# Performance work log

Measured on AMD Instinct MI355X. Metric: run time of the kernel, lower is better.

## Reference

```python
import jax, jax.numpy as jnp
import numpy as np

B, O, D = 4096, 256, 256  # batch, size_out (rules), size_in (features)


def setup_inputs() -> dict:
    key = jax.random.key(0)
    k1, k2, k3, k4, k5 = jax.random.split(key, 5)
    return {
        "x": jax.random.normal(k1, (B, D), dtype=jnp.float32),
        "scales": jax.random.normal(k2, (O, D), dtype=jnp.float32),
        # strict upper triangle holds the packed rot vectors (original inits them to zeros;
        # small values keep the quadratic form well conditioned)
        "rots": jax.random.normal(k3, (O, D, D), dtype=jnp.float32) * 0.02,
        "centroids": jax.random.normal(k4, (O, D, 1), dtype=jnp.float32),
        "b": jax.random.uniform(k5, (O,), dtype=jnp.float32, minval=0.5, maxval=1.5),
    }


def reference(x, scales, rots, centroids, b):
    # Build symmetric transform A[o] = diag(scales[o]) + triu(rots[o],1) + triu(rots[o],1)^T
    # (equivalent to the loop of diag_embed(r_i, i+1) + mirrored lower diagonal).
    upper = jnp.triu(rots, 1)                                   # [O,D,D]
    A = upper + jnp.swapaxes(upper, -1, -2)
    A = A + jnp.eye(D, dtype=scales.dtype) * scales[:, None, :]  # diag_embed(scales)
    # Augmented affine map: mul[o,i,b'] = A[o] @ x[b'] + centroid[o,i]; const row dropped
    # since only the first size_in rows feed the norm.
    y = jnp.einsum('bj,oij->boi', x, A) + centroids[..., 0][None, :, :]  # [B,O,D]
    rx = jnp.sqrt(jnp.sum(y * y, axis=-1))                      # L2 norm over D -> [B,O]
    return 1.0 / (1.0 + rx ** (2.0 * b))                        # bell membership [B,O]
```

## Files before the change

### kernel.cpp

```cpp
#include <hip/hip_runtime.h>
#include <cstdint>
#include <cmath>

#define Bn 4096
#define Dn 256
#define On 256

typedef __bf16 v8bf __attribute__((ext_vector_type(8)));
typedef float  v4f  __attribute__((ext_vector_type(4)));
typedef unsigned short us8 __attribute__((ext_vector_type(8)));

__device__ __forceinline__ unsigned short f2bf(float f) {
    unsigned int u = __builtin_bit_cast(unsigned int, f);
    unsigned int r = (u + 0x7fffu + ((u >> 16) & 1u)) >> 16;
    return (unsigned short)r;
}

__device__ __forceinline__ void gl_lds16(const void* g, void* l) {
    __builtin_amdgcn_global_load_lds(
        (const __attribute__((address_space(1))) void*)(uintptr_t)g,
        (__attribute__((address_space(3))) void*)(uintptr_t)l, 16, 0, 0);
}

__global__ __launch_bounds__(256) void prep(
    const float* __restrict__ scales, const float* __restrict__ rots,
    const float* __restrict__ x, unsigned short* __restrict__ Ap,
    unsigned short* __restrict__ xb) {
    const int bid = blockIdx.x;
    const int tid = threadIdx.x;

    if (bid >= 2560) {
        const int cb = bid - 2560;
#pragma unroll
        for (int s = 0; s < 4; ++s) {
            const int i = cb * 4096 + s * 1024 + tid * 4;
            const float4 v = *(const float4*)(x + i);
            ushort4 u;
            u.x = f2bf(v.x); u.y = f2bf(v.y); u.z = f2bf(v.z); u.w = f2bf(v.w);
            *(ushort4*)(xb + i) = u;
        }
        return;
    }

    static const int TI[10] = {0, 0, 0, 0, 1, 1, 1, 2, 2, 3};
    static const int TJ[10] = {0, 1, 2, 3, 1, 2, 3, 2, 3, 3};
    const int o  = bid / 10;
    const int p  = bid - o * 10;
    const int ti = TI[p], tj = TJ[p];

    __shared__ float t[64][68];
    const float* src = rots + (size_t)o * Dn * Dn + (size_t)(ti * 64) * Dn + tj * 64;
#pragma unroll
    for (int s = 0; s < 4; ++s) {
        const int idx = s * 256 + tid;
        const int r = idx >> 4, c = (idx & 15) * 4;
        const float4 v = *(const float4*)(src + r * Dn + c);
        *(float4*)&t[r][c] = v;
    }
    __syncthreads();

#pragma unroll
    for (int it = 0; it < 2; ++it) {
        const int slot = it * 256 + tid;
        const int bk = slot >> 6, L = slot & 63;
        const int quad = L >> 4, frow = L & 15;
        const int sl = bk >> 1, kl = bk & 1;
        const int r = sl * 16 + frow, c = kl * 32 + quad * 8;
        float v[8];
        if (ti == tj) {
#pragma unroll
            for (int q = 0; q < 8; ++q) {
                const int cc = c + q;
                v[q] = (r < cc) ? t[r][cc]
                     : ((r > cc) ? t[cc][r] : scales[o * Dn + ti * 64 + r]);
            }
        } else {
            const float4 a = *(const float4*)&t[r][c];
            const float4 b = *(const float4*)&t[r][c + 4];
            v[0] = a.x; v[1] = a.y; v[2] = a.z; v[3] = a.w;
            v[4] = b.x; v[5] = b.y; v[6] = b.z; v[7] = b.w;
        }
        us8 u;
#pragma unroll
        for (int q = 0; q < 8; ++q) u[q] = f2bf(v[q]);
        const size_t off = ((size_t)((o * 16 + ti * 4 + sl) * 8 + tj * 2 + kl)) * 512 + L * 8;
        *(us8*)(Ap + off) = u;
    }

    if (ti != tj) {
#pragma unroll
        for (int it = 0; it < 2; ++it) {
            const int slot = it * 256 + tid;
            const int bk = slot >> 6, L = slot & 63;
            const int quad = L >> 4, frow = L & 15;
            const int sl = bk >> 1, kl = bk & 1;
            const int r = sl * 16 + frow, c = kl * 32 + quad * 8;
            us8 u;
#pragma unroll
            for (int q = 0; q < 8; ++q) u[q] = f2bf(t[c + q][r]);
            const size_t off = ((size_t)((o * 16 + tj * 4 + sl) * 8 + ti * 2 + kl)) * 512 + L * 8;
            *(us8*)(Ap + off) = u;
        }
    }
}

__global__ __launch_bounds__(256, 3) void fuzzy_main(
    const unsigned short* __restrict__ Ap, const unsigned short* __restrict__ xb,
    const float* __restrict__ cent, const float* __restrict__ bvals,
    float* __restrict__ out) {
    __shared__ __align__(16) unsigned short Xs[4][64 * 64];
    __shared__ float ssbuf[4][64];
    __shared__ float centL[Dn];

    const int tid  = threadIdx.x;
    const int lane = tid & 63;
    const int wv   = tid >> 6;
    const int Lb = blockIdx.x;
    const int o  = (Lb & 7) * 32 + (Lb >> 9);
    const int b0 = ((Lb >> 3) & 63) * 64;

    centL[tid] = cent[o * Dn + tid];

    const int frow = lane & 15, quad = lane >> 4, f3 = lane & 7;
    const int lr = lane >> 3, ls = lane & 7;
    const int ksw = (ls ^ lr) * 8;

#pragma unroll
    for (int c = 0; c < 4; ++c)
#pragma unroll
        for (int q = 0; q < 2; ++q) {
            const int row = (wv * 2 + q) * 8 + lr;
            gl_lds16(xb + (size_t)(b0 + row) * Dn + c * 64 + ksw,
                     &Xs[c][row * 64 + ls * 8]);
        }

    const unsigned short* Aw = Ap + (size_t)(o * 16 + wv * 4) * 4096;

    v4f acc[4][4];
#pragma unroll
    for (int mi = 0; mi < 4; ++mi)
#pragma unroll
        for (int ni = 0; ni < 4; ++ni)
            acc[mi][ni] = v4f{0.f, 0.f, 0.f, 0.f};

    v8bf af[2][4];
#pragma unroll
    for (int mi = 0; mi < 4; ++mi)
        af[0][mi] = *(const v8bf*)(Aw + (size_t)mi * 8 * 512 + lane * 8);

    __syncthreads();

#pragma unroll
    for (int t = 0; t < 8; ++t) {
        const int cur = t & 1, nxt = cur ^ 1;
        if (t < 7) {
#pragma unroll
            for (int mi = 0; mi < 4; ++mi)
                af[nxt][mi] = *(const v8bf*)(Aw + (size_t)(mi * 8 + t + 1) * 512 + lane * 8);
        }
        v8bf xf[4];
        const int sl = ((t & 1) * 4 + quad) ^ f3;
#pragma unroll
        for (int ni = 0; ni < 4; ++ni)
            xf[ni] = *(const v8bf*)&Xs[t >> 1][(ni * 16 + frow) * 64 + sl * 8];
#pragma unroll
        for (int mi = 0; mi < 4; ++mi)
#pragma unroll
            for (int ni = 0; ni < 4; ++ni)
                acc[mi][ni] = __builtin_amdgcn_mfma_f32_16x16x32_bf16(
                    af[cur][mi], xf[ni], acc[mi][ni], 0, 0, 0);
    }

    float cv[4][4];
#pragma unroll
    for (int mi = 0; mi < 4; ++mi)
#pragma unroll
        for (int rg = 0; rg < 4; ++rg)
            cv[mi][rg] = centL[wv * 64 + mi * 16 + quad * 4 + rg];
#pragma unroll
    for (int ni = 0; ni < 4; ++ni) {
        float v = 0.f;
#pragma unroll
        for (int mi = 0; mi < 4; ++mi)
#pragma unroll
            for (int rg = 0; rg < 4; ++rg) {
                const float y = acc[mi][ni][rg] + cv[mi][rg];
                v += y * y;
            }
        v += __shfl_xor(v, 16);
        v += __shfl_xor(v, 32);
        if (lane < 16) {
            if (wv == 0) ssbuf[0][ni * 16 + lane] = v;
        }
    }
    __syncthreads();
    if (wv > 0) {
#pragma unroll
        for (int ni = 0; ni < 4; ++ni) {
            float v = 0.f;
#pragma unroll
            for (int mi = 0; mi < 4; ++mi)
#pragma unroll
                for (int rg = 0; rg < 4; ++rg) {
                    const float y = acc[mi][ni][rg] + cv[mi][rg];
                    v += y * y;
                }
            v += __shfl_xor(v, 16);
            v += __shfl_xor(v, 32);
            if (lane < 16) ssbuf[wv][ni * 16 + lane] = v;
        }
    }
    __syncthreads();
    if (tid < 64) {
        const float ssq = ssbuf[0][tid] + ssbuf[1][tid] + ssbuf[2][tid] + ssbuf[3][tid];
        out[(size_t)(b0 + tid) * On + o] = 1.0f / (1.0f + powf(ssq, bvals[o]));
    }
}

__global__ void fallback_kernel(const float* __restrict__ x, const float* __restrict__ scales,
                                const float* __restrict__ rots, const float* __restrict__ cent,
                                const float* __restrict__ bvals, float* __restrict__ out) {
    const int b = blockIdx.x * blockDim.x + threadIdx.x;
    const int o = blockIdx.y;
    if (b >= Bn) return;
    const float* R  = rots + (size_t)o * Dn * Dn;
    const float* xv = x + (size_t)b * Dn;
    float ss = 0.f;
    for (int i = 0; i < Dn; ++i) {
        float a = cent[o * Dn + i];
        for (int j = 0; j < Dn; ++j) {
            const float w = (j > i) ? R[i * Dn + j]
                          : ((j < i) ? R[j * Dn + i] : scales[o * Dn + i]);
            a += w * xv[j];
        }
        ss += a * a;
    }
    out[(size_t)b * On + o] = 1.f / (1.f + powf(ss, bvals[o]));
}

extern "C" void kernel_launch(void* const* d_in, const int* in_sizes, int n_in,
                              void* d_out, int out_size, void* d_ws, size_t ws_size,
                              hipStream_t stream) {
    const float* x         = (const float*)d_in[0];
    const float* scales    = (const float*)d_in[1];
    const float* rots      = (const float*)d_in[2];
    const float* centroids = (const float*)d_in[3];
    const float* bvals     = (const float*)d_in[4];
    float* out = (float*)d_out;

    const size_t needA = (size_t)On * Dn * Dn * sizeof(unsigned short);
    const size_t needX = (size_t)Bn * Dn * sizeof(unsigned short);

    if (ws_size >= needA + needX) {
        unsigned short* Ap = (unsigned short*)d_ws;
        unsigned short* xb = (unsigned short*)((char*)d_ws + needA);
        prep<<<dim3(2816), 256, 0, stream>>>(scales, rots, x, Ap, xb);
        fuzzy_main<<<dim3(16384), 256, 0, stream>>>(Ap, xb, centroids, bvals, out);
    } else {
        fallback_kernel<<<dim3(Bn / 256, On), 256, 0, stream>>>(x, scales, rots, centroids,
                                                                bvals, out);
    }
}
```

Before: 252.9 us.

## Keep A tile in registers and loop over batch tiles with double-buffered X

The main kernel now launches 512 long-lived blocks instead of 16384 short ones. Each block loads its rule's bf16 A fragments into registers once, then iterates over 32 batch tiles of 64 rows. The next X tile is prefetched into a second LDS buffer while the current one feeds the MFMAs. This removes the repeated reloading of A from L2/HBM for every batch tile, which is the main memory cost. In exchange, holding the whole A slice needs many VGPRs, so occupancy drops to 2 blocks per CU and latency hiding relies on a single barrier per iteration.

```diff
diff --git a/kernel.cpp b/kernel.cpp
--- a/kernel.cpp
+++ b/kernel.cpp
@@ -104,20 +104,20 @@
     }
 }
 
-__global__ __launch_bounds__(256, 3) void fuzzy_main(
+__global__ __launch_bounds__(256, 2) void fuzzy_main(
     const unsigned short* __restrict__ Ap, const unsigned short* __restrict__ xb,
     const float* __restrict__ cent, const float* __restrict__ bvals,
     float* __restrict__ out) {
-    __shared__ __align__(16) unsigned short Xs[4][64 * 64];
-    __shared__ float ssbuf[4][64];
+    __shared__ __align__(16) unsigned short Xs[2][4][64 * 64];
+    __shared__ float ssbuf[2][4][64];
     __shared__ float centL[Dn];
 
     const int tid  = threadIdx.x;
     const int lane = tid & 63;
     const int wv   = tid >> 6;
     const int Lb = blockIdx.x;
-    const int o  = (Lb & 7) * 32 + (Lb >> 9);
-    const int b0 = ((Lb >> 3) & 63) * 64;
+    const int o     = (Lb & 7) * 32 + ((Lb >> 3) & 31);
+    const int bhalf = Lb >> 8;
 
     centL[tid] = cent[o * Dn + tid];
 
@@ -125,76 +125,71 @@
     const int lr = lane >> 3, ls = lane & 7;
     const int ksw = (ls ^ lr) * 8;
 
-#pragma unroll
-    for (int c = 0; c < 4; ++c)
-#pragma unroll
-        for (int q = 0; q < 2; ++q) {
-            const int row = (wv * 2 + q) * 8 + lr;
-            gl_lds16(xb + (size_t)(b0 + row) * Dn + c * 64 + ksw,
-                     &Xs[c][row * 64 + ls * 8]);
-        }
-
     const unsigned short* Aw = Ap + (size_t)(o * 16 + wv * 4) * 4096;
-
-    v4f acc[4][4];
+    v8bf af[4][8];
 #pragma unroll
     for (int mi = 0; mi < 4; ++mi)
 #pragma unroll
-        for (int ni = 0; ni < 4; ++ni)
-            acc[mi][ni] = v4f{0.f, 0.f, 0.f, 0.f};
-
-    v8bf af[2][4];
+        for (int t = 0; t < 8; ++t)
+            af[mi][t] = *(const v8bf*)(Aw + (size_t)(mi * 8 + t) * 512 + lane * 8);
+
+    float cv[4][4];
 #pragma unroll
     for (int mi = 0; mi < 4; ++mi)
-        af[0][mi] = *(const v8bf*)(Aw + (size_t)mi * 8 * 512 + lane * 8);
-
+#pragma unroll
+        for (int rg = 0; rg < 4; ++rg)
+            cv[mi][rg] = cent[o * Dn + wv * 64 + mi * 16 + quad * 4 + rg];
+
+    {
+        const int b0 = bhalf * 2048;
+#pragma unroll
+        for (int c = 0; c < 4; ++c)
+#pragma unroll
+            for (int q = 0; q < 2; ++q) {
+                const int row = (wv * 2 + q) * 8 + lr;
+                gl_lds16(xb + (size_t)(b0 + row) * Dn + c * 64 + ksw,
+                         &Xs[0][c][row * 64 + ls * 8]);
+            }
+    }
     __syncthreads();
 
-#pragma unroll
-    for (int t = 0; t < 8; ++t) {
-        const int cur = t & 1, nxt = cur ^ 1;
-        if (t < 7) {
+    for (int it = 0; it < 32; ++it) {
+        const int buf = it & 1;
+        const int b0  = bhalf * 2048 + it * 64;
+        if (it < 31) {
+            const int nb0 = b0 + 64;
+#pragma unroll
+            for (int c = 0; c < 4; ++c)
+#pragma unroll
+                for (int q = 0; q < 2; ++q) {
+                    const int row = (wv * 2 + q) * 8 + lr;
+                    gl_lds16(xb + (size_t)(nb0 + row) * Dn + c * 64 + ksw,
+                             &Xs[buf ^ 1][c][row * 64 + ls * 8]);
+                }
+        }
+
+        v4f acc[4][4];
+#pragma unroll
+        for (int mi = 0; mi < 4; ++mi)
+#pragma unroll
+            for (int ni = 0; ni < 4; ++ni)
+                acc[mi][ni] = v4f{0.f, 0.f, 0.f, 0.f};
+
+#pragma unroll
+        for (int t = 0; t < 8; ++t) {
+            v8bf xf[4];
+            const int sl = ((t & 1) * 4 + quad) ^ f3;
+#pragma unroll
+            for (int ni = 0; ni < 4; ++ni)
+                xf[ni] = *(const v8bf*)&Xs[buf][t >> 1][(ni * 16 + frow) * 64 + sl * 8];
 #pragma unroll
             for (int mi = 0; mi < 4; ++mi)
-                af[nxt][mi] = *(const v8bf*)(Aw + (size_t)(mi * 8 + t + 1) * 512 + lane * 8);
-        }
-        v8bf xf[4];
-        const int sl = ((t & 1) * 4 + quad) ^ f3;
-#pragma unroll
-        for (int ni = 0; ni < 4; ++ni)
-            xf[ni] = *(const v8bf*)&Xs[t >> 1][(ni * 16 + frow) * 64 + sl * 8];
-#pragma unroll
-        for (int mi = 0; mi < 4; ++mi)
-#pragma unroll
-            for (int ni = 0; ni < 4; ++ni)
-                acc[mi][ni] = __builtin_amdgcn_mfma_f32_16x16x32_bf16(
-                    af[cur][mi], xf[ni], acc[mi][ni], 0, 0, 0);
-    }
-
-    float cv[4][4];
-#pragma unroll
-    for (int mi = 0; mi < 4; ++mi)
-#pragma unroll
-        for (int rg = 0; rg < 4; ++rg)
-            cv[mi][rg] = centL[wv * 64 + mi * 16 + quad * 4 + rg];
-#pragma unroll
-    for (int ni = 0; ni < 4; ++ni) {
-        float v = 0.f;
-#pragma unroll
-        for (int mi = 0; mi < 4; ++mi)
-#pragma unroll
-            for (int rg = 0; rg < 4; ++rg) {
-                const float y = acc[mi][ni][rg] + cv[mi][rg];
-                v += y * y;
-            }
-        v += __shfl_xor(v, 16);
-        v += __shfl_xor(v, 32);
-        if (lane < 16) {
-            if (wv == 0) ssbuf[0][ni * 16 + lane] = v;
-        }
-    }
-    __syncthreads();
-    if (wv > 0) {
+#pragma unroll
+                for (int ni = 0; ni < 4; ++ni)
+                    acc[mi][ni] = __builtin_amdgcn_mfma_f32_16x16x32_bf16(
+                        af[mi][t], xf[ni], acc[mi][ni], 0, 0, 0);
+        }
+
 #pragma unroll
         for (int ni = 0; ni < 4; ++ni) {
             float v = 0.f;
@@ -207,13 +202,14 @@
                 }
             v += __shfl_xor(v, 16);
             v += __shfl_xor(v, 32);
-            if (lane < 16) ssbuf[wv][ni * 16 + lane] = v;
-        }
-    }
-    __syncthreads();
-    if (tid < 64) {
-        const float ssq = ssbuf[0][tid] + ssbuf[1][tid] + ssbuf[2][tid] + ssbuf[3][tid];
-        out[(size_t)(b0 + tid) * On + o] = 1.0f / (1.0f + powf(ssq, bvals[o]));
+            if (lane < 16) ssbuf[buf][wv][ni * 16 + lane] = v;
+        }
+        __syncthreads();
+        if (tid < 64) {
+            const float ssq = ssbuf[buf][0][tid] + ssbuf[buf][1][tid] +
+                              ssbuf[buf][2][tid] + ssbuf[buf][3][tid];
+            out[(size_t)(b0 + tid) * On + o] = 1.0f / (1.0f + powf(ssq, bvals[o]));
+        }
     }
 }
 
@@ -255,7 +251,7 @@
         unsigned short* Ap = (unsigned short*)d_ws;
         unsigned short* xb = (unsigned short*)((char*)d_ws + needA);
         prep<<<dim3(2816), 256, 0, stream>>>(scales, rots, x, Ap, xb);
-        fuzzy_main<<<dim3(16384), 256, 0, stream>>>(Ap, xb, centroids, bvals, out);
+        fuzzy_main<<<dim3(512), 256, 0, stream>>>(Ap, xb, centroids, bvals, out);
     } else {
         fallback_kernel<<<dim3(Bn / 256, On), 256, 0, stream>>>(x, scales, rots, centroids,
                                                                 bvals, out);
```

Measured after the change: 215.0 us. -15.0%, faster.
